# Optimization experiments

Measured on AMD Instinct MI355X. Metric: run time of the kernel, lower is better.

The kernel has to match this reference:

```python
import jax, jax.numpy as jnp
import numpy as np

B, S, D, H = 4, 2048, 1024, 16
HD = D // H  # head_dim = 64


def setup_inputs() -> dict:
    key = jax.random.key(0)
    kx, kq, kk, kv, ko = jax.random.split(key, 5)
    scale = 1.0 / np.sqrt(D)
    return {
        "x": jax.random.normal(kx, (B, S, D), dtype=jnp.float32),
        "Wq": jax.random.normal(kq, (D, D), dtype=jnp.float32) * scale,
        "Wk": jax.random.normal(kk, (D, D), dtype=jnp.float32) * scale,
        "Wv": jax.random.normal(kv, (D, D), dtype=jnp.float32) * scale,
        "Wo": jax.random.normal(ko, (D, D), dtype=jnp.float32) * scale,
    }


def reference(x, Wq, Wk, Wv, Wo):
    b, s, d = x.shape
    # torch nn.Linear: y = x @ W.T
    q = (x @ Wq.T).reshape(b, s, H, HD).transpose(0, 2, 1, 3)  # [B,H,S,hd]
    k = (x @ Wk.T).reshape(b, s, H, HD).transpose(0, 2, 1, 3)
    v = (x @ Wv.T).reshape(b, s, H, HD).transpose(0, 2, 1, 3)
    attn = jnp.einsum("bhqd,bhkd->bhqk", q, k) / np.sqrt(HD)  # [B,H,S,S]
    attn = jax.nn.softmax(attn, axis=-1)
    out = jnp.einsum("bhqk,bhkd->bhqd", attn, v)  # [B,H,S,hd]
    per_head = out.transpose(0, 2, 1, 3)  # [B,S,H,hd]
    combined = per_head.reshape(b, s, d)
    projected = combined @ Wo.T
    return projected, per_head
```

## Files before the change

### kernel.cpp

```cpp
#include <hip/hip_runtime.h>
#include <hip/hip_bf16.h>

#define BB 4
#define SS 2048
#define DD 1024
#define HH 16
#define HDD 64
#define MM (BB*SS)

using bf16x8  = __attribute__((ext_vector_type(8))) short;
using f32x4   = __attribute__((ext_vector_type(4))) float;
using f32x16  = __attribute__((ext_vector_type(16))) float;
using ushort8 = __attribute__((ext_vector_type(8))) unsigned short;
using ushort4v= __attribute__((ext_vector_type(4))) unsigned short;
using uint4v  = __attribute__((ext_vector_type(4))) unsigned int;

#if __has_builtin(__builtin_amdgcn_exp2f)
#define EXP2(x) __builtin_amdgcn_exp2f(x)
#else
#define EXP2(x) exp2f(x)
#endif

__device__ __forceinline__ unsigned short f2bf(float x) {
    unsigned u = __builtin_bit_cast(unsigned, x);
    u += 0x7FFFu + ((u >> 16) & 1u);
    return (unsigned short)(u >> 16);
}

__device__ __forceinline__ unsigned int cvtpk(float lo, float hi) {
    unsigned int r;
    asm("v_cvt_pk_bf16_f32 %0, %1, %2" : "=v"(r) : "v"(lo), "v"(hi));
    return r;
}

#define PSWAP(a, b) asm("v_permlane32_swap_b32 %0, %1" : "+v"(a), "+v"(b))

__device__ __forceinline__ void load_lds16(const void* g, void* l) {
    __builtin_amdgcn_global_load_lds(
        (const __attribute__((address_space(1))) void*)g,
        (__attribute__((address_space(3))) void*)l, 16, 0, 0);
}

__global__ __launch_bounds__(256) void cvt_bf16(const float* __restrict__ in,
                                                unsigned short* __restrict__ out,
                                                int n, float scale) {
    int i = (blockIdx.x * 256 + threadIdx.x) * 8;
    if (i >= n) return;
    float4 a = *(const float4*)(in + i);
    float4 b = *(const float4*)(in + i + 4);
    ushort8 r;
    r[0] = f2bf(a.x*scale); r[1] = f2bf(a.y*scale); r[2] = f2bf(a.z*scale); r[3] = f2bf(a.w*scale);
    r[4] = f2bf(b.x*scale); r[5] = f2bf(b.y*scale); r[6] = f2bf(b.z*scale); r[7] = f2bf(b.w*scale);
    *(ushort8*)(out + i) = r;
}

__global__ __launch_bounds__(256) void cvt_weights(const float* __restrict__ wq,
                                                   const float* __restrict__ wk,
                                                   const float* __restrict__ wv,
                                                   const float* __restrict__ wo,
                                                   unsigned short* __restrict__ oq,
                                                   unsigned short* __restrict__ ok,
                                                   unsigned short* __restrict__ ov,
                                                   unsigned short* __restrict__ oo) {
    const int z = blockIdx.y;
    const float* src = z == 0 ? wq : z == 1 ? wk : z == 2 ? wv : wo;
    unsigned short* dst = z == 0 ? oq : z == 1 ? ok : z == 2 ? ov : oo;
    const float scale = z == 0 ? 0.18033688011112042f : 1.0f;
    int i = (blockIdx.x * 256 + threadIdx.x) * 8;
    float4 a = *(const float4*)(src + i);
    float4 b = *(const float4*)(src + i + 4);
    ushort8 r;
    r[0] = f2bf(a.x*scale); r[1] = f2bf(a.y*scale); r[2] = f2bf(a.z*scale); r[3] = f2bf(a.w*scale);
    r[4] = f2bf(b.x*scale); r[5] = f2bf(b.y*scale); r[6] = f2bf(b.z*scale); r[7] = f2bf(b.w*scale);
    *(ushort8*)(dst + i) = r;
}

template<int LAYOUT>
__device__ __forceinline__ void gemm_body(const unsigned short* __restrict__ A,
                                          const unsigned short* __restrict__ W,
                                          void* __restrict__ Cout,
                                          unsigned short* As ,
                                          unsigned short* Bs) {
    const int t    = threadIdx.x;
    const int lane = t & 63, wid = t >> 6;
    const int wr   = wid >> 1, wc = wid & 1;
    const int lrow = lane & 15, lkg = lane >> 4;
    const int lid  = blockIdx.y * 8 + blockIdx.x;
    const int ord  = (lid & 7) * 64 + (lid >> 3);
    const int row0 = (ord >> 3) * 128, col0 = (ord & 7) * 128;

    f32x4 acc[4][4];
    #pragma unroll
    for (int m = 0; m < 4; ++m)
        #pragma unroll
        for (int n = 0; n < 4; ++n) acc[m][n] = (f32x4){0.f, 0.f, 0.f, 0.f};

    const int c0 = t, c1 = t + 256;
    const unsigned short* Ag0 = A + (size_t)(row0 + (c0 >> 2)) * DD + (c0 & 3) * 8;
    const unsigned short* Ag1 = A + (size_t)(row0 + (c1 >> 2)) * DD + (c1 & 3) * 8;
    const unsigned short* Wg0 = W + (size_t)(col0 + (c0 >> 2)) * DD + (c0 & 3) * 8;
    const unsigned short* Wg1 = W + (size_t)(col0 + (c1 >> 2)) * DD + (c1 & 3) * 8;

    auto stage = [&](int buf, int k0) {
        load_lds16(Ag0 + k0, &As[buf*128*32 + c0 * 8]);
        load_lds16(Ag1 + k0, &As[buf*128*32 + c1 * 8]);
        load_lds16(Wg0 + k0, &Bs[buf*128*32 + c0 * 8]);
        load_lds16(Wg1 + k0, &Bs[buf*128*32 + c1 * 8]);
    };

    stage(0, 0);
    __syncthreads();
    for (int kt = 0; kt < DD / 32; ++kt) {
        const int cur = kt & 1;
        if (kt + 1 < DD / 32) stage(cur ^ 1, (kt + 1) * 32);
        bf16x8 af[4], bfr[4];
        #pragma unroll
        for (int m = 0; m < 4; ++m)
            af[m] = *(const bf16x8*)&As[cur*128*32 + (wr*64 + m*16 + lrow) * 32 + lkg*8];
        #pragma unroll
        for (int n = 0; n < 4; ++n)
            bfr[n] = *(const bf16x8*)&Bs[cur*128*32 + (wc*64 + n*16 + lrow) * 32 + lkg*8];
        __builtin_amdgcn_s_setprio(1);
        #pragma unroll
        for (int m = 0; m < 4; ++m)
            #pragma unroll
            for (int n = 0; n < 4; ++n)
                acc[m][n] = __builtin_amdgcn_mfma_f32_16x16x32_bf16(af[m], bfr[n], acc[m][n], 0, 0, 0);
        __builtin_amdgcn_s_setprio(0);
        __syncthreads();
    }

    #pragma unroll
    for (int m = 0; m < 4; ++m) {
        #pragma unroll
        for (int n = 0; n < 4; ++n) {
            if (LAYOUT == 2) {
                int gm0 = row0 + wr*64 + m*16 + lkg*4;
                int gn  = col0 + wc*64 + n*16 + lrow;
                int b_ = gm0 >> 11, s0 = gm0 & 2047;
                int h_ = gn >> 6,  hd = gn & 63;
                ushort4v hv;
                hv[0] = f2bf(acc[m][n][0]); hv[1] = f2bf(acc[m][n][1]);
                hv[2] = f2bf(acc[m][n][2]); hv[3] = f2bf(acc[m][n][3]);
                *(ushort4v*)&((unsigned short*)Cout)[(((size_t)b_*HH + h_)*HDD + hd)*SS + s0] = hv;
            } else {
                #pragma unroll
                for (int j = 0; j < 4; ++j) {
                    int gm = row0 + wr*64 + m*16 + lkg*4 + j;
                    int gn = col0 + wc*64 + n*16 + lrow;
                    float v = acc[m][n][j];
                    if (LAYOUT == 1) {
                        int b_ = gm >> 11, s_ = gm & 2047;
                        int h_ = gn >> 6,  hd = gn & 63;
                        ((unsigned short*)Cout)[(((size_t)b_*HH + h_)*SS + s_)*HDD + hd] = f2bf(v);
                    } else {
                        ((float*)Cout)[(size_t)gm * DD + gn] = v;
                    }
                }
            }
        }
    }
}

__global__ __launch_bounds__(256) void gemm_qkv(const unsigned short* __restrict__ A,
                                                const unsigned short* __restrict__ Wq,
                                                const unsigned short* __restrict__ Wk,
                                                const unsigned short* __restrict__ Wv,
                                                unsigned short* __restrict__ Q,
                                                unsigned short* __restrict__ K,
                                                unsigned short* __restrict__ V) {
    __shared__ unsigned short As[2*128*32];
    __shared__ unsigned short Bs[2*128*32];
    const int z = blockIdx.z;
    if (z == 2)      gemm_body<2>(A, Wv, V, As, Bs);
    else if (z == 1) gemm_body<1>(A, Wk, K, As, Bs);
    else             gemm_body<1>(A, Wq, Q, As, Bs);
}

__global__ __launch_bounds__(256) void gemm_proj(const unsigned short* __restrict__ A,
                                                 const unsigned short* __restrict__ W,
                                                 float* __restrict__ C) {
    __shared__ unsigned short As[2*128*32];
    __shared__ unsigned short Bs[2*128*32];
    gemm_body<0>(A, W, C, As, Bs);
}

__global__ __launch_bounds__(256) void flash_mfma6(const unsigned short* __restrict__ Qg,
                                                   const unsigned short* __restrict__ Kg,
                                                   const unsigned short* __restrict__ Vtg,
                                                   float* __restrict__ outf,
                                                   unsigned short* __restrict__ outb) {
    __shared__ unsigned short Ks[2][64*64];
    __shared__ unsigned short Vs[2][64*64];
    const int t   = threadIdx.x, lane = t & 63, wid = t >> 6;
    const int l31 = lane & 31;
    const int hi  = lane >> 5;
    const int lid = blockIdx.y * 16 + blockIdx.x;
    const int ord = (lid & 7) * 128 + (lid >> 3);
    const int bh  = ord >> 4, b_ = bh >> 4, h_ = bh & 15;
    const int q0  = (ord & 15) * 128 + wid * 32;

    const unsigned short* Qb = Qg  + (size_t)bh * SS * HDD;
    const unsigned short* Kb = Kg  + (size_t)bh * SS * HDD;
    const unsigned short* Vb = Vtg + (size_t)bh * HDD * SS;

    bf16x8 qf[4];
    #pragma unroll
    for (int ks = 0; ks < 4; ++ks)
        qf[ks] = *(const bf16x8*)&Qb[(size_t)(q0 + l31) * HDD + ks*16 + hi*8];

    f32x16 os0, os1;
    #pragma unroll
    for (int r = 0; r < 16; ++r) { os0[r] = 0.f; os1[r] = 0.f; }
    float lsum = 0.f;

    const int c0 = t, c1 = t + 256;
    const unsigned sb0 = ((unsigned)(c0 << 4)) ^ ((((unsigned)c0 >> 3) & 7u) << 4);
    const unsigned sb1 = ((unsigned)(c1 << 4)) ^ ((((unsigned)c1 >> 3) & 7u) << 4);
    const unsigned xs  = ((unsigned)(l31 & 7)) << 4;

    bf16x8 kr0, kr1, vr0, vr1;
    kr0 = *(const bf16x8*)&Kb[8*c0];
    kr1 = *(const bf16x8*)&Kb[8*c1];
    vr0 = *(const bf16x8*)&Vb[(size_t)(c0 >> 3) * SS + (c0 & 7) * 8];
    vr1 = *(const bf16x8*)&Vb[(size_t)(c1 >> 3) * SS + (c1 & 7) * 8];
    *(bf16x8*)((char*)&Ks[0][0] + sb0) = kr0;
    *(bf16x8*)((char*)&Ks[0][0] + sb1) = kr1;
    *(bf16x8*)((char*)&Vs[0][0] + sb0) = vr0;
    *(bf16x8*)((char*)&Vs[0][0] + sb1) = vr1;
    __syncthreads();

    for (int kt = 0; kt < SS/64; ++kt) {
        const int cur = kt & 1;
        if (kt + 1 < SS/64) {
            kr0 = *(const bf16x8*)&Kb[(size_t)(kt+1)*4096 + 8*c0];
            kr1 = *(const bf16x8*)&Kb[(size_t)(kt+1)*4096 + 8*c1];
            vr0 = *(const bf16x8*)&Vb[(size_t)(c0 >> 3) * SS + (kt+1)*64 + (c0 & 7) * 8];
            vr1 = *(const bf16x8*)&Vb[(size_t)(c1 >> 3) * SS + (kt+1)*64 + (c1 & 7) * 8];
        }
        const char* Kc = (const char*)&Ks[cur][0];
        const char* Vc = (const char*)&Vs[cur][0];

        f32x16 sa0, sa1;
        #pragma unroll
        for (int r = 0; r < 16; ++r) { sa0[r] = 0.f; sa1[r] = 0.f; }
        __builtin_amdgcn_s_setprio(1);
        #pragma unroll
        for (int ks = 0; ks < 4; ++ks) {
            const unsigned cb = ks*32 + hi*16;
            bf16x8 kf0 = *(const bf16x8*)(Kc + (((unsigned)(l31*128)      + cb) ^ xs));
            bf16x8 kf1 = *(const bf16x8*)(Kc + (((unsigned)((32+l31)*128) + cb) ^ xs));
            sa0 = __builtin_amdgcn_mfma_f32_32x32x16_bf16(kf0, qf[ks], sa0, 0, 0, 0);
            sa1 = __builtin_amdgcn_mfma_f32_32x32x16_bf16(kf1, qf[ks], sa1, 0, 0, 0);
        }
        __builtin_amdgcn_s_setprio(0);

        float rsa = 0.f, rsb = 0.f, rsc = 0.f, rsd = 0.f;
        #pragma unroll
        for (int r = 0; r < 16; r += 4) {
            sa0[r]   = EXP2(sa0[r]);   rsa += sa0[r];
            sa0[r+1] = EXP2(sa0[r+1]); rsb += sa0[r+1];
            sa0[r+2] = EXP2(sa0[r+2]); rsc += sa0[r+2];
            sa0[r+3] = EXP2(sa0[r+3]); rsd += sa0[r+3];
        }
        #pragma unroll
        for (int r = 0; r < 16; r += 4) {
            sa1[r]   = EXP2(sa1[r]);   rsa += sa1[r];
            sa1[r+1] = EXP2(sa1[r+1]); rsb += sa1[r+1];
            sa1[r+2] = EXP2(sa1[r+2]); rsc += sa1[r+2];
            sa1[r+3] = EXP2(sa1[r+3]); rsd += sa1[r+3];
        }
        lsum += (rsa + rsb) + (rsc + rsd);

        unsigned int pk0[4][2], pk1[4][2];
        #pragma unroll
        for (int a = 0; a < 4; ++a) {
            #pragma unroll
            for (int h = 0; h < 2; ++h) {
                pk0[a][h] = cvtpk(sa0[4*a + 2*h], sa0[4*a + 2*h + 1]);
                pk1[a][h] = cvtpk(sa1[4*a + 2*h], sa1[4*a + 2*h + 1]);
            }
        }

        __builtin_amdgcn_s_setprio(1);
        #pragma unroll
        for (int ksg = 0; ksg < 4; ++ksg) {
            const int ks2 = (ksg & 1) * 2;
            unsigned int w0, w1, w2, w3;
            if ((ksg >> 1) == 0) {
                w0 = pk0[ks2][0];   w2 = pk0[ks2+1][0];
                w1 = pk0[ks2][1];   w3 = pk0[ks2+1][1];
            } else {
                w0 = pk1[ks2][0];   w2 = pk1[ks2+1][0];
                w1 = pk1[ks2][1];   w3 = pk1[ks2+1][1];
            }
            PSWAP(w0, w2);
            PSWAP(w1, w3);
            uint4v wv = {w0, w1, w2, w3};
            bf16x8 pf = __builtin_bit_cast(bf16x8, wv);
            const unsigned cb = ksg*32 + hi*16;
            bf16x8 vf0 = *(const bf16x8*)(Vc + (((unsigned)(l31*128)      + cb) ^ xs));
            bf16x8 vf1 = *(const bf16x8*)(Vc + (((unsigned)((32+l31)*128) + cb) ^ xs));
            os0 = __builtin_amdgcn_mfma_f32_32x32x16_bf16(vf0, pf, os0, 0, 0, 0);
            os1 = __builtin_amdgcn_mfma_f32_32x32x16_bf16(vf1, pf, os1, 0, 0, 0);
        }
        __builtin_amdgcn_s_setprio(0);

        if (kt + 1 < SS/64) {
            char* Kn = (char*)&Ks[cur ^ 1][0];
            char* Vn = (char*)&Vs[cur ^ 1][0];
            *(bf16x8*)(Kn + sb0) = kr0;
            *(bf16x8*)(Kn + sb1) = kr1;
            *(bf16x8*)(Vn + sb0) = vr0;
            *(bf16x8*)(Vn + sb1) = vr1;
        }
        __syncthreads();
    }

    const float L    = lsum + __shfl_xor(lsum, 32);
    const float invl = 1.0f / L;
    const int   s_   = q0 + l31;
    float*          po = outf + (((size_t)b_ * SS + s_) * HH + h_) * HDD;
    unsigned short* pb = outb + (((size_t)b_ * SS + s_) * HH + h_) * HDD;
    #pragma unroll
    for (int a = 0; a < 4; ++a) {
        {
            const int d0 = 8*a + 4*hi;
            float4 v; v.x = os0[4*a+0]*invl; v.y = os0[4*a+1]*invl;
                      v.z = os0[4*a+2]*invl; v.w = os0[4*a+3]*invl;
            *(float4*)&po[d0] = v;
            ushort4v hv; hv[0]=f2bf(v.x); hv[1]=f2bf(v.y); hv[2]=f2bf(v.z); hv[3]=f2bf(v.w);
            *(ushort4v*)&pb[d0] = hv;
        }
        {
            const int d0 = 32 + 8*a + 4*hi;
            float4 v; v.x = os1[4*a+0]*invl; v.y = os1[4*a+1]*invl;
                      v.z = os1[4*a+2]*invl; v.w = os1[4*a+3]*invl;
            *(float4*)&po[d0] = v;
            ushort4v hv; hv[0]=f2bf(v.x); hv[1]=f2bf(v.y); hv[2]=f2bf(v.z); hv[3]=f2bf(v.w);
            *(ushort4v*)&pb[d0] = hv;
        }
    }
}

extern "C" void kernel_launch(void* const* d_in, const int* in_sizes, int n_in,
                              void* d_out, int out_size, void* d_ws, size_t ws_size,
                              hipStream_t stream) {
    const float* x  = (const float*)d_in[0];
    const float* Wq = (const float*)d_in[1];
    const float* Wk = (const float*)d_in[2];
    const float* Wv = (const float*)d_in[3];
    const float* Wo = (const float*)d_in[4];
    float* out      = (float*)d_out;
    float* per_head = out + (size_t)MM * DD;

    unsigned short* ws   = (unsigned short*)d_ws;
    const size_t NE = (size_t)MM * DD;
    unsigned short* Qbf  = ws;
    unsigned short* Kbf  = Qbf + NE;
    unsigned short* Vbf  = Kbf + NE;
    unsigned short* xbf  = Vbf + NE;
    unsigned short* wqbf = xbf + NE;
    unsigned short* wkbf = wqbf + (size_t)DD * DD;
    unsigned short* wvbf = wkbf + (size_t)DD * DD;
    unsigned short* wobf = wvbf + (size_t)DD * DD;
    unsigned short* cbf  = wobf + (size_t)DD * DD;

    const int nx = MM * DD;
    const int nw = DD * DD;
    cvt_bf16<<<nx / 2048, 256, 0, stream>>>(x, xbf, nx, 1.0f);
    cvt_weights<<<dim3(nw / 2048, 4), 256, 0, stream>>>(Wq, Wk, Wv, Wo,
                                                        wqbf, wkbf, wvbf, wobf);

    dim3 gg(DD / 128, MM / 128);
    gemm_qkv<<<dim3(DD / 128, MM / 128, 3), 256, 0, stream>>>(xbf, wqbf, wkbf, wvbf,
                                                              Qbf, Kbf, Vbf);

    flash_mfma6<<<dim3(SS / 128, BB * HH), 256, 0, stream>>>(Qbf, Kbf, Vbf, per_head, cbf);

    gemm_proj<<<gg, 256, 0, stream>>>(cbf, wobf, out);
}
```

Before: 209.2 us.

## Process two query tiles per wave and compute row sums via MFMA

Each workgroup now handles 256 query rows instead of 128: every wave holds two 32-row Q fragments and reuses each K/V LDS fragment for both. This halves K/V global and LDS traffic per query row. The softmax row sum moves from scalar adds to an extra MFMA against a vector of ones, which takes VALU work off the critical path. The cost is much higher register pressure (four output accumulators plus two sum accumulators), now bounded by launch_bounds(256,2), and half as many workgroups, which lowers parallelism.

```diff
diff --git a/kernel.cpp b/kernel.cpp
--- a/kernel.cpp
+++ b/kernel.cpp
@@ -79,8 +79,7 @@
 __device__ __forceinline__ void gemm_body(const unsigned short* __restrict__ A,
                                           const unsigned short* __restrict__ W,
                                           void* __restrict__ Cout,
-                                          unsigned short* As ,
-                                          unsigned short* Bs) {
+                                          unsigned short* As, unsigned short* Bs) {
     const int t    = threadIdx.x;
     const int lane = t & 63, wid = t >> 6;
     const int wr   = wid >> 1, wc = wid & 1;
@@ -185,34 +184,42 @@
     gemm_body<0>(A, W, C, As, Bs);
 }
 
-__global__ __launch_bounds__(256) void flash_mfma6(const unsigned short* __restrict__ Qg,
-                                                   const unsigned short* __restrict__ Kg,
-                                                   const unsigned short* __restrict__ Vtg,
-                                                   float* __restrict__ outf,
-                                                   unsigned short* __restrict__ outb) {
+__global__ __launch_bounds__(256, 2) void flash_mfma7(const unsigned short* __restrict__ Qg,
+                                                      const unsigned short* __restrict__ Kg,
+                                                      const unsigned short* __restrict__ Vtg,
+                                                      float* __restrict__ outf,
+                                                      unsigned short* __restrict__ outb) {
     __shared__ unsigned short Ks[2][64*64];
     __shared__ unsigned short Vs[2][64*64];
     const int t   = threadIdx.x, lane = t & 63, wid = t >> 6;
     const int l31 = lane & 31;
     const int hi  = lane >> 5;
-    const int lid = blockIdx.y * 16 + blockIdx.x;
-    const int ord = (lid & 7) * 128 + (lid >> 3);
-    const int bh  = ord >> 4, b_ = bh >> 4, h_ = bh & 15;
-    const int q0  = (ord & 15) * 128 + wid * 32;
+    const int lid = blockIdx.y * 8 + blockIdx.x;
+    const int ord = (lid & 7) * 64 + (lid >> 3);
+    const int bh  = ord >> 3, b_ = bh >> 4, h_ = bh & 15;
+    const int qA  = (ord & 7) * 256 + wid * 32;
 
     const unsigned short* Qb = Qg  + (size_t)bh * SS * HDD;
     const unsigned short* Kb = Kg  + (size_t)bh * SS * HDD;
     const unsigned short* Vb = Vtg + (size_t)bh * HDD * SS;
 
-    bf16x8 qf[4];
-    #pragma unroll
-    for (int ks = 0; ks < 4; ++ks)
-        qf[ks] = *(const bf16x8*)&Qb[(size_t)(q0 + l31) * HDD + ks*16 + hi*8];
-
-    f32x16 os0, os1;
-    #pragma unroll
-    for (int r = 0; r < 16; ++r) { os0[r] = 0.f; os1[r] = 0.f; }
-    float lsum = 0.f;
+    bf16x8 qfA[4], qfB[4];
+    #pragma unroll
+    for (int ks = 0; ks < 4; ++ks) {
+        qfA[ks] = *(const bf16x8*)&Qb[(size_t)(qA + l31) * HDD + ks*16 + hi*8];
+        qfB[ks] = *(const bf16x8*)&Qb[(size_t)(qA + 128 + l31) * HDD + ks*16 + hi*8];
+    }
+
+    f32x16 osA0, osA1, osB0, osB1, sumA, sumB, z;
+    #pragma unroll
+    for (int r = 0; r < 16; ++r) {
+        osA0[r] = 0.f; osA1[r] = 0.f; osB0[r] = 0.f; osB1[r] = 0.f;
+        sumA[r] = 0.f; sumB[r] = 0.f; z[r] = 0.f;
+    }
+
+    bf16x8 onesf;
+    #pragma unroll
+    for (int e = 0; e < 8; ++e) onesf[e] = (short)0x3F80;
 
     const int c0 = t, c1 = t + 256;
     const unsigned sb0 = ((unsigned)(c0 << 4)) ^ ((((unsigned)c0 >> 3) & 7u) << 4);
@@ -241,44 +248,36 @@
         const char* Kc = (const char*)&Ks[cur][0];
         const char* Vc = (const char*)&Vs[cur][0];
 
-        f32x16 sa0, sa1;
-        #pragma unroll
-        for (int r = 0; r < 16; ++r) { sa0[r] = 0.f; sa1[r] = 0.f; }
+        f32x16 saA0, saA1, saB0, saB1;
         __builtin_amdgcn_s_setprio(1);
         #pragma unroll
         for (int ks = 0; ks < 4; ++ks) {
             const unsigned cb = ks*32 + hi*16;
             bf16x8 kf0 = *(const bf16x8*)(Kc + (((unsigned)(l31*128)      + cb) ^ xs));
             bf16x8 kf1 = *(const bf16x8*)(Kc + (((unsigned)((32+l31)*128) + cb) ^ xs));
-            sa0 = __builtin_amdgcn_mfma_f32_32x32x16_bf16(kf0, qf[ks], sa0, 0, 0, 0);
-            sa1 = __builtin_amdgcn_mfma_f32_32x32x16_bf16(kf1, qf[ks], sa1, 0, 0, 0);
+            if (ks == 0) {
+                saA0 = __builtin_amdgcn_mfma_f32_32x32x16_bf16(kf0, qfA[0], z, 0, 0, 0);
+                saA1 = __builtin_amdgcn_mfma_f32_32x32x16_bf16(kf1, qfA[0], z, 0, 0, 0);
+                saB0 = __builtin_amdgcn_mfma_f32_32x32x16_bf16(kf0, qfB[0], z, 0, 0, 0);
+                saB1 = __builtin_amdgcn_mfma_f32_32x32x16_bf16(kf1, qfB[0], z, 0, 0, 0);
+            } else {
+                saA0 = __builtin_amdgcn_mfma_f32_32x32x16_bf16(kf0, qfA[ks], saA0, 0, 0, 0);
+                saA1 = __builtin_amdgcn_mfma_f32_32x32x16_bf16(kf1, qfA[ks], saA1, 0, 0, 0);
+                saB0 = __builtin_amdgcn_mfma_f32_32x32x16_bf16(kf0, qfB[ks], saB0, 0, 0, 0);
+                saB1 = __builtin_amdgcn_mfma_f32_32x32x16_bf16(kf1, qfB[ks], saB1, 0, 0, 0);
+            }
         }
         __builtin_amdgcn_s_setprio(0);
 
-        float rsa = 0.f, rsb = 0.f, rsc = 0.f, rsd = 0.f;
-        #pragma unroll
-        for (int r = 0; r < 16; r += 4) {
-            sa0[r]   = EXP2(sa0[r]);   rsa += sa0[r];
-            sa0[r+1] = EXP2(sa0[r+1]); rsb += sa0[r+1];
-            sa0[r+2] = EXP2(sa0[r+2]); rsc += sa0[r+2];
-            sa0[r+3] = EXP2(sa0[r+3]); rsd += sa0[r+3];
-        }
-        #pragma unroll
-        for (int r = 0; r < 16; r += 4) {
-            sa1[r]   = EXP2(sa1[r]);   rsa += sa1[r];
-            sa1[r+1] = EXP2(sa1[r+1]); rsb += sa1[r+1];
-            sa1[r+2] = EXP2(sa1[r+2]); rsc += sa1[r+2];
-            sa1[r+3] = EXP2(sa1[r+3]); rsd += sa1[r+3];
-        }
-        lsum += (rsa + rsb) + (rsc + rsd);
-
-        unsigned int pk0[4][2], pk1[4][2];
+        unsigned int pkA0[4][2], pkA1[4][2], pkB0[4][2], pkB1[4][2];
         #pragma unroll
         for (int a = 0; a < 4; ++a) {
             #pragma unroll
             for (int h = 0; h < 2; ++h) {
-                pk0[a][h] = cvtpk(sa0[4*a + 2*h], sa0[4*a + 2*h + 1]);
-                pk1[a][h] = cvtpk(sa1[4*a + 2*h], sa1[4*a + 2*h + 1]);
+                pkA0[a][h] = cvtpk(EXP2(saA0[4*a + 2*h]), EXP2(saA0[4*a + 2*h + 1]));
+                pkA1[a][h] = cvtpk(EXP2(saA1[4*a + 2*h]), EXP2(saA1[4*a + 2*h + 1]));
+                pkB0[a][h] = cvtpk(EXP2(saB0[4*a + 2*h]), EXP2(saB0[4*a + 2*h + 1]));
+                pkB1[a][h] = cvtpk(EXP2(saB1[4*a + 2*h]), EXP2(saB1[4*a + 2*h + 1]));
             }
         }
 
@@ -286,23 +285,29 @@
         #pragma unroll
         for (int ksg = 0; ksg < 4; ++ksg) {
             const int ks2 = (ksg & 1) * 2;
-            unsigned int w0, w1, w2, w3;
+            unsigned int a0, a1, a2, a3, b0, b1, b2, b3;
             if ((ksg >> 1) == 0) {
-                w0 = pk0[ks2][0];   w2 = pk0[ks2+1][0];
-                w1 = pk0[ks2][1];   w3 = pk0[ks2+1][1];
+                a0 = pkA0[ks2][0]; a2 = pkA0[ks2+1][0]; a1 = pkA0[ks2][1]; a3 = pkA0[ks2+1][1];
+                b0 = pkB0[ks2][0]; b2 = pkB0[ks2+1][0]; b1 = pkB0[ks2][1]; b3 = pkB0[ks2+1][1];
             } else {
-                w0 = pk1[ks2][0];   w2 = pk1[ks2+1][0];
-                w1 = pk1[ks2][1];   w3 = pk1[ks2+1][1];
-            }
-            PSWAP(w0, w2);
-            PSWAP(w1, w3);
-            uint4v wv = {w0, w1, w2, w3};
-            bf16x8 pf = __builtin_bit_cast(bf16x8, wv);
+                a0 = pkA1[ks2][0]; a2 = pkA1[ks2+1][0]; a1 = pkA1[ks2][1]; a3 = pkA1[ks2+1][1];
+                b0 = pkB1[ks2][0]; b2 = pkB1[ks2+1][0]; b1 = pkB1[ks2][1]; b3 = pkB1[ks2+1][1];
+            }
+            PSWAP(a0, a2); PSWAP(a1, a3);
+            PSWAP(b0, b2); PSWAP(b1, b3);
+            uint4v wa = {a0, a1, a2, a3};
+            uint4v wb = {b0, b1, b2, b3};
+            bf16x8 pfA = __builtin_bit_cast(bf16x8, wa);
+            bf16x8 pfB = __builtin_bit_cast(bf16x8, wb);
             const unsigned cb = ksg*32 + hi*16;
             bf16x8 vf0 = *(const bf16x8*)(Vc + (((unsigned)(l31*128)      + cb) ^ xs));
             bf16x8 vf1 = *(const bf16x8*)(Vc + (((unsigned)((32+l31)*128) + cb) ^ xs));
-            os0 = __builtin_amdgcn_mfma_f32_32x32x16_bf16(vf0, pf, os0, 0, 0, 0);
-            os1 = __builtin_amdgcn_mfma_f32_32x32x16_bf16(vf1, pf, os1, 0, 0, 0);
+            osA0 = __builtin_amdgcn_mfma_f32_32x32x16_bf16(vf0, pfA, osA0, 0, 0, 0);
+            osA1 = __builtin_amdgcn_mfma_f32_32x32x16_bf16(vf1, pfA, osA1, 0, 0, 0);
+            osB0 = __builtin_amdgcn_mfma_f32_32x32x16_bf16(vf0, pfB, osB0, 0, 0, 0);
+            osB1 = __builtin_amdgcn_mfma_f32_32x32x16_bf16(vf1, pfB, osB1, 0, 0, 0);
+            sumA = __builtin_amdgcn_mfma_f32_32x32x16_bf16(onesf, pfA, sumA, 0, 0, 0);
+            sumB = __builtin_amdgcn_mfma_f32_32x32x16_bf16(onesf, pfB, sumB, 0, 0, 0);
         }
         __builtin_amdgcn_s_setprio(0);
 
@@ -317,28 +322,32 @@
         __syncthreads();
     }
 
-    const float L    = lsum + __shfl_xor(lsum, 32);
-    const float invl = 1.0f / L;
-    const int   s_   = q0 + l31;
-    float*          po = outf + (((size_t)b_ * SS + s_) * HH + h_) * HDD;
-    unsigned short* pb = outb + (((size_t)b_ * SS + s_) * HH + h_) * HDD;
-    #pragma unroll
-    for (int a = 0; a < 4; ++a) {
-        {
-            const int d0 = 8*a + 4*hi;
-            float4 v; v.x = os0[4*a+0]*invl; v.y = os0[4*a+1]*invl;
-                      v.z = os0[4*a+2]*invl; v.w = os0[4*a+3]*invl;
-            *(float4*)&po[d0] = v;
-            ushort4v hv; hv[0]=f2bf(v.x); hv[1]=f2bf(v.y); hv[2]=f2bf(v.z); hv[3]=f2bf(v.w);
-            *(ushort4v*)&pb[d0] = hv;
-        }
-        {
-            const int d0 = 32 + 8*a + 4*hi;
-            float4 v; v.x = os1[4*a+0]*invl; v.y = os1[4*a+1]*invl;
-                      v.z = os1[4*a+2]*invl; v.w = os1[4*a+3]*invl;
-            *(float4*)&po[d0] = v;
-            ushort4v hv; hv[0]=f2bf(v.x); hv[1]=f2bf(v.y); hv[2]=f2bf(v.z); hv[3]=f2bf(v.w);
-            *(ushort4v*)&pb[d0] = hv;
+    #pragma unroll
+    for (int g = 0; g < 2; ++g) {
+        const float invl = 1.0f / (g == 0 ? sumA[0] : sumB[0]);
+        const int   s_   = qA + (g ? 128 : 0) + l31;
+        float*          po = outf + (((size_t)b_ * SS + s_) * HH + h_) * HDD;
+        unsigned short* pb = outb + (((size_t)b_ * SS + s_) * HH + h_) * HDD;
+        #pragma unroll
+        for (int a = 0; a < 4; ++a) {
+            {
+                const f32x16& o = g == 0 ? osA0 : osB0;
+                const int d0 = 8*a + 4*hi;
+                float4 v; v.x = o[4*a+0]*invl; v.y = o[4*a+1]*invl;
+                          v.z = o[4*a+2]*invl; v.w = o[4*a+3]*invl;
+                *(float4*)&po[d0] = v;
+                ushort4v hv; hv[0]=f2bf(v.x); hv[1]=f2bf(v.y); hv[2]=f2bf(v.z); hv[3]=f2bf(v.w);
+                *(ushort4v*)&pb[d0] = hv;
+            }
+            {
+                const f32x16& o = g == 0 ? osA1 : osB1;
+                const int d0 = 32 + 8*a + 4*hi;
+                float4 v; v.x = o[4*a+0]*invl; v.y = o[4*a+1]*invl;
+                          v.z = o[4*a+2]*invl; v.w = o[4*a+3]*invl;
+                *(float4*)&po[d0] = v;
+                ushort4v hv; hv[0]=f2bf(v.x); hv[1]=f2bf(v.y); hv[2]=f2bf(v.z); hv[3]=f2bf(v.w);
+                *(ushort4v*)&pb[d0] = hv;
+            }
         }
     }
 }
@@ -372,11 +381,10 @@
     cvt_weights<<<dim3(nw / 2048, 4), 256, 0, stream>>>(Wq, Wk, Wv, Wo,
                                                         wqbf, wkbf, wvbf, wobf);
 
-    dim3 gg(DD / 128, MM / 128);
     gemm_qkv<<<dim3(DD / 128, MM / 128, 3), 256, 0, stream>>>(xbf, wqbf, wkbf, wvbf,
                                                               Qbf, Kbf, Vbf);
 
-    flash_mfma6<<<dim3(SS / 128, BB * HH), 256, 0, stream>>>(Qbf, Kbf, Vbf, per_head, cbf);
-
-    gemm_proj<<<gg, 256, 0, stream>>>(cbf, wobf, out);
-}
+    flash_mfma7<<<dim3(8, BB * HH), 256, 0, stream>>>(Qbf, Kbf, Vbf, per_head, cbf);
+
+    gemm_proj<<<dim3(DD / 128, MM / 128), 256, 0, stream>>>(cbf, wobf, out);
+}
```

Measured after the change: 192.8 us. 7.8% less time.
